# Kernel tuning notes

Measured on AMD Instinct MI355X. Metric: run time of the kernel, lower is better.

Reference implementation:

```python
import jax, jax.numpy as jnp
import numpy as np

UNITS = 256  # intr_dim


def _lstm_scan(x, W, U, b):
    """Keras-style LSTM (gate order i,f,c,o), return last hidden state.
    x: [B,T,D], W: [D,4H], U: [H,4H], b: [4H] -> h_last [B,H]"""
    B = x.shape[0]
    H = U.shape[0]
    # precompute input projections for all timesteps: [T,B,4H]
    xw = jnp.einsum('btd,dg->tbg', x, W) + b

    def step(carry, xw_t):
        h, c = carry
        z = xw_t + h @ U  # [B,4H]
        i = jax.nn.sigmoid(z[:, :H])
        f = jax.nn.sigmoid(z[:, H:2 * H])
        g = jnp.tanh(z[:, 2 * H:3 * H])
        o = jax.nn.sigmoid(z[:, 3 * H:])
        c_new = f * c + i * g
        h_new = o * jnp.tanh(c_new)
        return (h_new, c_new), None

    init = (jnp.zeros((B, H), x.dtype), jnp.zeros((B, H), x.dtype))
    (h_last, _), _ = jax.lax.scan(step, init, xw)
    return h_last


def setup_inputs() -> dict:
    key = jax.random.key(0)
    ks = jax.random.split(key, 6)
    B, T, D, H = 64, 2048, 256, UNITS
    s = 1.0 / np.sqrt(D)
    sr = 1.0 / np.sqrt(H)
    return {
        'x': jax.random.normal(ks[0], (B, T, D), jnp.float32),
        'Wf': jax.random.normal(ks[1], (D, 4 * H), jnp.float32) * s,
        'Uf': jax.random.normal(ks[2], (H, 4 * H), jnp.float32) * sr,
        'bf': jnp.zeros((4 * H,), jnp.float32),
        'Wb': jax.random.normal(ks[3], (D, 4 * H), jnp.float32) * s,
        'Ub': jax.random.normal(ks[4], (H, 4 * H), jnp.float32) * sr,
        'bb': jnp.zeros((4 * H,), jnp.float32),
    }


def reference(x, Wf, Uf, bf, Wb, Ub, bb):
    # Bidirectional LSTM, return_sequences=False, merge_mode='concat'.
    # Recurrent dropout and output Dropout are identity at inference.
    h_fwd = _lstm_scan(x, Wf, Uf, bf)
    h_bwd = _lstm_scan(x[:, ::-1, :], Wb, Ub, bb)
    return jnp.concatenate([h_fwd, h_bwd], axis=-1)  # [B, 2H]
```

## Files before the change

kernel.cpp:

```cpp
#include <hip/hip_runtime.h>

#define T_TOTAL 2048

typedef short bf16x8 __attribute__((ext_vector_type(8)));
typedef float f32x4 __attribute__((ext_vector_type(4)));

#define OFF_WT  0ull
#define OFF_UT  (1ull<<20)
#define OFF_HG  (2ull<<20)
#define OFF_HFR (OFF_HG + (128ull<<10))
#define OFF_CST (OFF_HG + (192ull<<10))
#define OFF_CTR (OFF_HG + (256ull<<10))
#define OFF_XW  (3ull<<20)
#define STEP_BYTES 262144ull

__device__ __forceinline__ unsigned short f2bf(float f){
  unsigned int u = __builtin_bit_cast(unsigned int, f);
  u += 0x7fffu + ((u>>16)&1u);
  return (unsigned short)(u>>16);
}
__device__ __forceinline__ float bfhi2f(unsigned int u){
  unsigned int v = u & 0xffff0000u; return __builtin_bit_cast(float, v);
}
__device__ __forceinline__ float bflo2f(unsigned int u){
  unsigned int v = u << 16; return __builtin_bit_cast(float, v);
}
__device__ __forceinline__ float sigf(float z){ return 1.0f/(1.0f + __expf(-z)); }
__device__ __forceinline__ float tanhf_(float z){ return 2.0f/(1.0f + __expf(-2.0f*z)) - 1.0f; }

__global__ __launch_bounds__(256) void kprep(const float* __restrict__ Wf, const float* __restrict__ Uf,
                                             const float* __restrict__ Wb, const float* __restrict__ Ub,
                                             unsigned short* __restrict__ ws){
  __shared__ float tile[64][65];
  int mat = blockIdx.z;
  const float* src = (mat==0)?Wf:(mat==1)?Wb:(mat==2)?Uf:Ub;
  unsigned short* dst = ws + ((mat<2)?0u:524288u) + (unsigned)(mat&1)*262144u;
  int c0 = blockIdx.x*64, k0 = blockIdx.y*64;
  int tx = threadIdx.x & 63, ty = threadIdx.x >> 6;
  #pragma unroll
  for (int j=0;j<16;j++){
    int r = j*4+ty;
    tile[r][tx] = src[(size_t)(k0+r)*1024 + (c0+tx)];
  }
  __syncthreads();
  #pragma unroll
  for (int j=0;j<16;j++){
    int r = j*4+ty;
    int col = c0+r, k = k0+tx;
    int cg = col>>4, ks = k>>5, kq = (k>>3)&3, e = k&7;
    dst[(size_t)(cg*8+ks)*512 + ((col&15)+16*kq)*8 + e] = f2bf(tile[tx][r]);
  }
}

__global__ __launch_bounds__(512) void kgemm(const float* __restrict__ x,
        const float* __restrict__ biasF, const float* __restrict__ biasB,
        const unsigned short* __restrict__ wsu, char* __restrict__ xw,
        int s0, int Tthis){
  __shared__ __align__(16) char smem[147456];
  char* abuf = smem + 131072;
  int chunk = blockIdx.x, dir = blockIdx.y, q = blockIdx.z;
  int tid = threadIdx.x, w = tid>>6, l = tid&63;
  int l15 = l&15;
  const char* WT = (const char*)(wsu + (size_t)dir*262144u);
  const float* bias = dir ? biasB : biasF;

  bf16x8 wfrA[8][4];
  bf16x8 wfrV[8][2];
  #pragma unroll
  for (int ct=0;ct<8;ct++){
    int cg = 8*w + ct;
    const char* base = WT + (size_t)cg*8192 + (size_t)l*16;
    #pragma unroll
    for (int ks=0;ks<4;ks++) wfrA[ct][ks] = *(const bf16x8*)(base + ks*1024);
    wfrV[ct][0] = *(const bf16x8*)(base + 4*1024);
    wfrV[ct][1] = *(const bf16x8*)(base + 5*1024);
    #pragma unroll
    for (int k2=0;k2<2;k2++){
      bf16x8 t = *(const bf16x8*)(base + (6+k2)*1024);
      *(bf16x8*)(smem + ((cg*2+k2)*1024 + l*16)) = t;
    }
  }
  float bv[8];
  #pragma unroll
  for (int ct=0;ct<8;ct++) bv[ct] = bias[128*w + ct*16 + l15];

  int b_loc = tid>>5, kk = (tid&31)*8;
  int b = q*16 + b_loc;
  int aslot = (kk>>5)*1024 + (b_loc + 16*((kk>>3)&3))*16;

  int nt = Tthis - chunk*64; if (nt > 64) nt = 64; if (nt < 0) nt = 0;
  if (nt > 0){
    int sg = s0 + chunk*64;
    int t_src = dir ? (T_TOTAL-1-sg) : sg;
    const float* px = x + ((size_t)b*T_TOTAL + t_src)*256 + kk;
    float4 v0 = *(const float4*)px;
    float4 v1 = *(const float4*)(px+4);
    uint4 pk;
    pk.x = (unsigned)f2bf(v0.x) | ((unsigned)f2bf(v0.y)<<16);
    pk.y = (unsigned)f2bf(v0.z) | ((unsigned)f2bf(v0.w)<<16);
    pk.z = (unsigned)f2bf(v1.x) | ((unsigned)f2bf(v1.y)<<16);
    pk.w = (unsigned)f2bf(v1.z) | ((unsigned)f2bf(v1.w)<<16);
    *(uint4*)(abuf + aslot) = pk;
  }
  __syncthreads();

  int p = 0;
  for (int tl=0; tl<nt; ++tl){
    float4 v0, v1;
    int have_next = (tl+1 < nt);
    if (have_next){
      int sg = s0 + chunk*64 + tl + 1;
      int t_src = dir ? (T_TOTAL-1-sg) : sg;
      const float* px = x + ((size_t)b*T_TOTAL + t_src)*256 + kk;
      v0 = *(const float4*)px;
      v1 = *(const float4*)(px+4);
    }
    char* outp = xw + (size_t)(chunk*64+tl)*STEP_BYTES + (size_t)dir*131072u + (size_t)q*32768u;
    #pragma unroll
    for (int half=0; half<2; ++half){
      f32x4 acc[4];
      #pragma unroll
      for (int ci=0;ci<4;ci++){
        float b0 = bv[half*4+ci];
        acc[ci][0]=b0; acc[ci][1]=b0; acc[ci][2]=b0; acc[ci][3]=b0;
      }
      #pragma unroll
      for (int ks=0;ks<4;ks++){
        bf16x8 a = *(const bf16x8*)(abuf + p*8192 + ks*1024 + l*16);
        #pragma unroll
        for (int ci=0;ci<4;ci++)
          acc[ci] = __builtin_amdgcn_mfma_f32_16x16x32_bf16(a, wfrA[half*4+ci][ks], acc[ci], 0, 0, 0);
      }
      #pragma unroll
      for (int k2=0;k2<2;k2++){
        bf16x8 a = *(const bf16x8*)(abuf + p*8192 + (4+k2)*1024 + l*16);
        #pragma unroll
        for (int ci=0;ci<4;ci++)
          acc[ci] = __builtin_amdgcn_mfma_f32_16x16x32_bf16(a, wfrV[half*4+ci][k2], acc[ci], 0, 0, 0);
      }
      #pragma unroll
      for (int k2=0;k2<2;k2++){
        bf16x8 a = *(const bf16x8*)(abuf + p*8192 + (6+k2)*1024 + l*16);
        #pragma unroll
        for (int ci=0;ci<4;ci++){
          bf16x8 bb = *(const bf16x8*)(smem + (((8*w+half*4+ci)*2+k2)*1024 + l*16));
          acc[ci] = __builtin_amdgcn_mfma_f32_16x16x32_bf16(a, bb, acc[ci], 0, 0, 0);
        }
      }
      #pragma unroll
      for (int ci=0;ci<4;ci++){
        int col = 128*w + (half*4+ci)*16 + l15;
        uint2 pk;
        pk.x = (unsigned)f2bf(acc[ci][0]) | ((unsigned)f2bf(acc[ci][1])<<16);
        pk.y = (unsigned)f2bf(acc[ci][2]) | ((unsigned)f2bf(acc[ci][3])<<16);
        *(uint2*)(outp + (size_t)col*32 + (l>>4)*8) = pk;
      }
    }
    if (have_next){
      uint4 pk;
      pk.x = (unsigned)f2bf(v0.x) | ((unsigned)f2bf(v0.y)<<16);
      pk.y = (unsigned)f2bf(v0.z) | ((unsigned)f2bf(v0.w)<<16);
      pk.z = (unsigned)f2bf(v1.x) | ((unsigned)f2bf(v1.y)<<16);
      pk.w = (unsigned)f2bf(v1.z) | ((unsigned)f2bf(v1.w)<<16);
      *(uint4*)(abuf + (p^1)*8192 + aslot) = pk;
    }
    __syncthreads();
    p ^= 1;
  }
}

__global__ __launch_bounds__(512) void krec(const unsigned short* __restrict__ wsu,
        const char* __restrict__ xw, char* __restrict__ hg, char* __restrict__ hfr,
        float* __restrict__ cst, unsigned int* __restrict__ flags,
        float* __restrict__ out, int nsteps, int s0, int last){
  __shared__ __align__(16) char Bl[131072];
  __shared__ __align__(16) char Ab[16384];
  int bid = blockIdx.x;
  int hs = bid>>3, dir = (bid>>2)&1, bq = bid&3;
  int tid = threadIdx.x, w = tid>>6, l = tid&63;
  int l15 = l&15;
  const char* UT = (const char*)(wsu + 524288u + (size_t)dir*262144u);

  bf16x8 Bf[2][8];
  #pragma unroll
  for (int g=0; g<2; g++){
    int cg = g*16 + hs*8 + w;
    #pragma unroll
    for (int ks=0;ks<8;ks++)
      Bf[g][ks] = *(const bf16x8*)(UT + (size_t)(cg*8+ks)*1024 + (size_t)l*16);
  }
  #pragma unroll
  for (int g=2; g<4; g++){
    int cg = g*16 + hs*8 + w;
    #pragma unroll
    for (int ks=0;ks<8;ks++){
      bf16x8 t = *(const bf16x8*)(UT + (size_t)(cg*8+ks)*1024 + (size_t)l*16);
      *(bf16x8*)(Bl + ((w*2+(g-2))*8+ks)*1024 + l*16) = t;
    }
  }

  unsigned int* myflag = flags + bid*32;
  unsigned int* pflag  = flags + (bid^8)*32;
  char* hgreg = hg + (size_t)(dir*4+bq)*16384u;

  int jh = w*16 + l15;
  int ksl = jh>>5, kqh = (jh>>3)&3, eh = jh&7;
  int jfull = hs*128 + jh;
  int bg = l>>4;

  float c_[4];
  if (s0 == 0){
    #pragma unroll
    for (int r=0;r<4;r++) c_[r] = 0.0f;
    *(uint4*)(Ab + tid*16) = make_uint4(0u,0u,0u,0u);
  } else {
    *(uint4*)(Ab + tid*16) = *(const uint4*)(hfr + (size_t)(dir*4+bq)*8192u + tid*16);
    #pragma unroll
    for (int r=0;r<4;r++)
      c_[r] = cst[((size_t)dir*64 + bq*16 + bg*4 + r)*256 + jfull];
  }
  __syncthreads();

  const char* XW = xw + (size_t)dir*131072u + (size_t)bq*32768u;
  uint2 xv[4];
  #pragma unroll
  for (int g=0;g<4;g++){
    int col = g*256 + hs*128 + w*16 + l15;
    xv[g] = *(const uint2*)(XW + (size_t)col*32 + bg*8);
  }

  for (int lt=0; lt<nsteps; ++lt){
    int par = lt&1;
    f32x4 acc[4];
    #pragma unroll
    for (int g=0;g<4;g++){
      uint2 v = xv[g];
      acc[g][0]=bflo2f(v.x); acc[g][1]=bfhi2f(v.x);
      acc[g][2]=bflo2f(v.y); acc[g][3]=bfhi2f(v.y);
    }
    #pragma unroll
    for (int ks=0;ks<8;ks++){
      bf16x8 a = *(const bf16x8*)(Ab + par*8192 + ks*1024 + l*16);
      acc[0] = __builtin_amdgcn_mfma_f32_16x16x32_bf16(a, Bf[0][ks], acc[0], 0, 0, 0);
      acc[1] = __builtin_amdgcn_mfma_f32_16x16x32_bf16(a, Bf[1][ks], acc[1], 0, 0, 0);
      bf16x8 b2 = *(const bf16x8*)(Bl + ((w*2+0)*8+ks)*1024 + l*16);
      acc[2] = __builtin_amdgcn_mfma_f32_16x16x32_bf16(a, b2, acc[2], 0, 0, 0);
      bf16x8 b3 = *(const bf16x8*)(Bl + ((w*2+1)*8+ks)*1024 + l*16);
      acc[3] = __builtin_amdgcn_mfma_f32_16x16x32_bf16(a, b3, acc[3], 0, 0, 0);
    }
    float hv[4];
    #pragma unroll
    for (int r=0;r<4;r++){
      float ig = sigf(acc[0][r]);
      float fg = sigf(acc[1][r]);
      float gg = tanhf_(acc[2][r]);
      float og = sigf(acc[3][r]);
      float cn = fg*c_[r] + ig*gg;
      c_[r] = cn;
      hv[r] = og*tanhf_(cn);
    }

    if (lt == nsteps-1){
      if (last){
        #pragma unroll
        for (int r=0;r<4;r++)
          out[(size_t)(bq*16 + bg*4 + r)*512 + dir*256 + jfull] = hv[r];
      } else {
        char* hw = hfr + (size_t)(dir*4+bq)*8192u + hs*4096;
        #pragma unroll
        for (int r=0;r<4;r++)
          *(unsigned short*)(hw + ksl*1024 + (bg*4+r + 16*kqh)*16 + eh*2) = f2bf(hv[r]);
        #pragma unroll
        for (int r=0;r<4;r++)
          cst[((size_t)dir*64 + bq*16 + bg*4 + r)*256 + jfull] = c_[r];
      }
      break;
    }

    int parn = par^1;
    {
      char* al = Ab + parn*8192 + hs*4096;
      char* ag = hgreg + (size_t)parn*8192u + hs*4096;
      #pragma unroll
      for (int r=0;r<4;r++){
        unsigned short hb = f2bf(hv[r]);
        int off = ksl*1024 + (bg*4+r + 16*kqh)*16 + eh*2;
        *(unsigned short*)(al + off) = hb;
        __hip_atomic_store((unsigned short*)(ag + off), hb,
                           __ATOMIC_RELAXED, __HIP_MEMORY_SCOPE_AGENT);
      }
    }
    asm volatile("s_waitcnt vmcnt(0)" ::: "memory");
    __syncthreads();
    if (tid == 0)
      __hip_atomic_store(myflag, (unsigned)(lt+1),
                         __ATOMIC_RELAXED, __HIP_MEMORY_SCOPE_AGENT);
    {
      #pragma unroll
      for (int g=0;g<4;g++){
        int col = g*256 + hs*128 + w*16 + l15;
        xv[g] = *(const uint2*)(XW + (size_t)(lt+1)*STEP_BYTES + (size_t)col*32 + bg*8);
      }
    }
    if (tid == 0){
      unsigned want = (unsigned)(lt+1);
      while (__hip_atomic_load(pflag, __ATOMIC_RELAXED, __HIP_MEMORY_SCOPE_AGENT) < want)
        ;
    }
    __syncthreads();
    {
      const unsigned* src = (const unsigned*)(hgreg + (size_t)parn*8192u + (1-hs)*4096);
      unsigned d0 = __hip_atomic_load(src + 2*tid,     __ATOMIC_RELAXED, __HIP_MEMORY_SCOPE_AGENT);
      unsigned d1 = __hip_atomic_load(src + 2*tid + 1, __ATOMIC_RELAXED, __HIP_MEMORY_SCOPE_AGENT);
      unsigned* dstl = (unsigned*)(Ab + parn*8192 + (1-hs)*4096);
      dstl[2*tid]   = d0;
      dstl[2*tid+1] = d1;
    }
    __syncthreads();
  }
}

extern "C" void kernel_launch(void* const* d_in, const int* in_sizes, int n_in,
                              void* d_out, int out_size, void* d_ws, size_t ws_size,
                              hipStream_t stream){
  (void)in_sizes; (void)n_in; (void)out_size;
  const float* x   = (const float*)d_in[0];
  const float* Wf  = (const float*)d_in[1];
  const float* Uf  = (const float*)d_in[2];
  const float* bf_ = (const float*)d_in[3];
  const float* Wb  = (const float*)d_in[4];
  const float* Ub  = (const float*)d_in[5];
  const float* bb  = (const float*)d_in[6];
  float* out = (float*)d_out;
  char* ws = (char*)d_ws;
  unsigned short* wsu = (unsigned short*)ws;
  char* hg  = ws + OFF_HG;
  char* hfr = ws + OFF_HFR;
  float* cst = (float*)(ws + OFF_CST);
  unsigned int* flags = (unsigned int*)(ws + OFF_CTR);
  char* xwb = ws + OFF_XW;

  kprep<<<dim3(16,4,4), 256, 0, stream>>>(Wf, Uf, Wb, Ub, wsu);

  long long avail = (long long)ws_size - (long long)OFF_XW;
  int Tseg = (avail > 0) ? (int)(avail / (long long)STEP_BYTES) : 1;
  if (Tseg < 1) Tseg = 1;
  if (Tseg > T_TOTAL) Tseg = T_TOTAL;
  int nseg = (T_TOTAL + Tseg - 1)/Tseg;
  int s0 = 0;
  for (int seg=0; seg<nseg; ++seg){
    int Tthis = (T_TOTAL - s0 < Tseg) ? (T_TOTAL - s0) : Tseg;
    int nchunk = (Tthis + 63)/64;
    (void)hipMemsetAsync(flags, 0, 2048, stream);
    kgemm<<<dim3(nchunk,2,4), 512, 0, stream>>>(x, bf_, bb, wsu, xwb, s0, Tthis);
    krec<<<dim3(16), 512, 0, stream>>>(wsu, xwb, hg, hfr, cst, flags, out, Tthis, s0,
                                       (seg==nseg-1)?1:0);
    s0 += Tthis;
  }
}
```

Before: 6.864 ms.

## Overlap partner hidden-state wait with local-half recurrent MFMAs

Splits each step's recurrent matmul into the locally produced K half and the partner block's half. The local half and the next-step xw prefetch run before spinning on the partner flag, which hides part of the cross-block exchange latency. The global h publish is also coalesced: h is written to LDS, then copied to global with one 64-bit atomic store per thread instead of per-element 16-bit atomic stores. The trade-off is one extra barrier per step, and the last step now prefetches xw it does not use.

```diff
diff --git a/kernel.cpp b/kernel.cpp
--- a/kernel.cpp
+++ b/kernel.cpp
@@ -4,6 +4,7 @@
 
 typedef short bf16x8 __attribute__((ext_vector_type(8)));
 typedef float f32x4 __attribute__((ext_vector_type(4)));
+typedef unsigned long long ull;
 
 #define OFF_WT  0ull
 #define OFF_UT  (1ull<<20)
@@ -230,7 +231,7 @@
   }
 
   for (int lt=0; lt<nsteps; ++lt){
-    int par = lt&1;
+    int par = lt&1, parn = par^1;
     f32x4 acc[4];
     #pragma unroll
     for (int g=0;g<4;g++){
@@ -239,7 +240,39 @@
       acc[g][2]=bflo2f(v.y); acc[g][3]=bfhi2f(v.y);
     }
     #pragma unroll
-    for (int ks=0;ks<8;ks++){
+    for (int k2=0;k2<4;k2++){
+      int ks = 4*hs + k2;
+      bf16x8 a = *(const bf16x8*)(Ab + par*8192 + ks*1024 + l*16);
+      acc[0] = __builtin_amdgcn_mfma_f32_16x16x32_bf16(a, Bf[0][ks], acc[0], 0, 0, 0);
+      acc[1] = __builtin_amdgcn_mfma_f32_16x16x32_bf16(a, Bf[1][ks], acc[1], 0, 0, 0);
+      bf16x8 b2 = *(const bf16x8*)(Bl + ((w*2+0)*8+ks)*1024 + l*16);
+      acc[2] = __builtin_amdgcn_mfma_f32_16x16x32_bf16(a, b2, acc[2], 0, 0, 0);
+      bf16x8 b3 = *(const bf16x8*)(Bl + ((w*2+1)*8+ks)*1024 + l*16);
+      acc[3] = __builtin_amdgcn_mfma_f32_16x16x32_bf16(a, b3, acc[3], 0, 0, 0);
+    }
+    {
+      int ltn = (lt+1 < nsteps) ? (lt+1) : lt;
+      #pragma unroll
+      for (int g=0;g<4;g++){
+        int col = g*256 + hs*128 + w*16 + l15;
+        xv[g] = *(const uint2*)(XW + (size_t)ltn*STEP_BYTES + (size_t)col*32 + bg*8);
+      }
+    }
+    if (lt > 0){
+      if (tid == 0){
+        unsigned want = (unsigned)lt;
+        while (__hip_atomic_load(pflag, __ATOMIC_RELAXED, __HIP_MEMORY_SCOPE_AGENT) < want)
+          ;
+      }
+      __syncthreads();
+      ull v = __hip_atomic_load((const ull*)(hgreg + (size_t)par*8192u + (1-hs)*4096 + tid*8),
+                                __ATOMIC_RELAXED, __HIP_MEMORY_SCOPE_AGENT);
+      *(ull*)(Ab + par*8192 + (1-hs)*4096 + tid*8) = v;
+      __syncthreads();
+    }
+    #pragma unroll
+    for (int k2=0;k2<4;k2++){
+      int ks = 4*(1-hs) + k2;
       bf16x8 a = *(const bf16x8*)(Ab + par*8192 + ks*1024 + l*16);
       acc[0] = __builtin_amdgcn_mfma_f32_16x16x32_bf16(a, Bf[0][ks], acc[0], 0, 0, 0);
       acc[1] = __builtin_amdgcn_mfma_f32_16x16x32_bf16(a, Bf[1][ks], acc[1], 0, 0, 0);
@@ -277,46 +310,25 @@
       break;
     }
 
-    int parn = par^1;
     {
       char* al = Ab + parn*8192 + hs*4096;
-      char* ag = hgreg + (size_t)parn*8192u + hs*4096;
       #pragma unroll
       for (int r=0;r<4;r++){
         unsigned short hb = f2bf(hv[r]);
-        int off = ksl*1024 + (bg*4+r + 16*kqh)*16 + eh*2;
-        *(unsigned short*)(al + off) = hb;
-        __hip_atomic_store((unsigned short*)(ag + off), hb,
-                           __ATOMIC_RELAXED, __HIP_MEMORY_SCOPE_AGENT);
-      }
+        *(unsigned short*)(al + ksl*1024 + (bg*4+r + 16*kqh)*16 + eh*2) = hb;
+      }
+    }
+    __syncthreads();
+    {
+      ull pv = *(const ull*)(Ab + parn*8192 + hs*4096 + tid*8);
+      __hip_atomic_store((ull*)(hgreg + (size_t)parn*8192u + hs*4096 + tid*8), pv,
+                         __ATOMIC_RELAXED, __HIP_MEMORY_SCOPE_AGENT);
     }
     asm volatile("s_waitcnt vmcnt(0)" ::: "memory");
     __syncthreads();
     if (tid == 0)
       __hip_atomic_store(myflag, (unsigned)(lt+1),
                          __ATOMIC_RELAXED, __HIP_MEMORY_SCOPE_AGENT);
-    {
-      #pragma unroll
-      for (int g=0;g<4;g++){
-        int col = g*256 + hs*128 + w*16 + l15;
-        xv[g] = *(const uint2*)(XW + (size_t)(lt+1)*STEP_BYTES + (size_t)col*32 + bg*8);
-      }
-    }
-    if (tid == 0){
-      unsigned want = (unsigned)(lt+1);
-      while (__hip_atomic_load(pflag, __ATOMIC_RELAXED, __HIP_MEMORY_SCOPE_AGENT) < want)
-        ;
-    }
-    __syncthreads();
-    {
-      const unsigned* src = (const unsigned*)(hgreg + (size_t)parn*8192u + (1-hs)*4096);
-      unsigned d0 = __hip_atomic_load(src + 2*tid,     __ATOMIC_RELAXED, __HIP_MEMORY_SCOPE_AGENT);
-      unsigned d1 = __hip_atomic_load(src + 2*tid + 1, __ATOMIC_RELAXED, __HIP_MEMORY_SCOPE_AGENT);
-      unsigned* dstl = (unsigned*)(Ab + parn*8192 + (1-hs)*4096);
-      dstl[2*tid]   = d0;
-      dstl[2*tid+1] = d1;
-    }
-    __syncthreads();
   }
 }
 
```

New measurement: 11.90 ms. 73.4% more time.
